# Kernel optimization log

Measured on AMD Instinct MI355X. Metric: run time of the kernel, lower is better.

The kernel has to match this reference:

```python
import jax, jax.numpy as jnp
import numpy as np
from jax import lax

T, B, R = 128, 128, 512  # timesteps, batch_size, read_size


def setup_inputs() -> dict:
    key = jax.random.key(0)
    ks = jax.random.split(key, 5)
    return {
        "u":  jax.random.uniform(ks[0], (T, B, 1), dtype=jnp.float32),
        "d1": jax.random.uniform(ks[1], (T, B, 1), dtype=jnp.float32),
        "d2": jax.random.uniform(ks[2], (T, B, 1), dtype=jnp.float32),
        "v1": jax.random.normal(ks[3], (T, B, R), dtype=jnp.float32),
        "v2": jax.random.normal(ks[4], (T, B, R), dtype=jnp.float32),
    }


def _forward(u, d1, d2, v1, v2):
    # Stack-style neural memory: each step pushes two (strength, value) slots,
    # reads up to total strength u from the top of the stack, then pops strength u.
    Tn, Bn, _ = u.shape
    Rn = v1.shape[-1]
    nslots = 2 * Tn
    # Pre-allocated slot store; unused slots have S=0, V=0 and contribute exactly 0
    # to both the read summary and strength_used, matching the growing-list semantics.
    S0 = jnp.zeros((nslots, Bn, 1), dtype=u.dtype)
    V0 = jnp.zeros((nslots, Bn, Rn), dtype=v1.dtype)

    def step(carry, inp):
        S, V = carry
        u_t, d1_t, d2_t, v1_t, v2_t, t = inp
        # push(d1, d2, v1, v2)
        S = S.at[2 * t].set(d1_t).at[2 * t + 1].set(d2_t)
        V = V.at[2 * t].set(v1_t).at[2 * t + 1].set(v2_t)
        Srev = S[::-1]  # stack order: top (most recent) first
        Vrev = V[::-1]

        # read(u): sequential scan over slots with strength bookkeeping
        def read_step(c, sv):
            summary, used = c
            s_i, v_i = sv
            # NOTE: torch.max(u - strength_used) is a GLOBAL max over the (B,1)
            # tensor (0-dim scalar), faithfully reproduced here.
            scal = jnp.max(u_t - used)
            summary = summary + v_i * jnp.minimum(s_i, scal)
            return (summary, used + s_i), None

        (summary, _), _ = lax.scan(
            read_step,
            (jnp.zeros((Bn, Rn), u.dtype), jnp.zeros((Bn, 1), u.dtype)),
            (Srev, Vrev),
        )

        # pop(u): elementwise strength depletion, same slot order
        def pop_step(used, s_i):
            s_new = s_i - jnp.minimum(s_i, jnp.maximum(jnp.zeros_like(s_i), u_t - used))
            return used + s_i, s_new

        _, Srev_new = lax.scan(pop_step, jnp.zeros((Bn, 1), u.dtype), Srev)
        return (Srev_new[::-1], V), summary

    xs = (u, d1, d2, v1, v2, jnp.arange(Tn))
    (_, _), outs = lax.scan(step, (S0, V0), xs)
    return outs  # (T, B, R) read contents per step


def reference(u, d1, d2, v1, v2):
    return _forward(u, d1, d2, v1, v2)
```

## Files before the change

kernel.cpp:

```cpp
#include <hip/hip_runtime.h>
#include <hip/hip_bf16.h>
#include <math.h>

constexpr int T = 128;
constexpr int B = 128;
constexpr int R = 512;
constexpr int NS = 256;

typedef __attribute__((ext_vector_type(8))) short bf16x8;
typedef __attribute__((ext_vector_type(4))) float f32x4;

static __device__ __forceinline__ ushort f2bf(float f) {
    union { float f; unsigned u; } v; v.f = f;
    unsigned r = v.u + 0x7fffu + ((v.u >> 16) & 1u);
    return (ushort)(r >> 16);
}

__global__ __launch_bounds__(512) void weights(
    const float* __restrict__ u, const float* __restrict__ d1,
    const float* __restrict__ d2, ushort* __restrict__ w)
{
    const int t    = blockIdx.x;
    const int tid  = threadIdx.x;
    const int wv   = tid >> 6;
    const int lane = tid & 63;
    __shared__ float eH[T][B];
    __shared__ float smin[8][B];

    const int nfl = t * B;
    for (int i = tid * 4; i < nfl; i += 2048) {
        const float4 a  = *(const float4*)(d1 + i);
        const float4 b4 = *(const float4*)(d2 + i);
        const float4 c4 = *(const float4*)(u + i);
        *(float4*)(&eH[0][0] + i) =
            make_float4(a.x + b4.x - c4.x, a.y + b4.y - c4.y,
                        a.z + b4.z - c4.z, a.w + b4.w - c4.w);
    }
    __syncthreads();

    if (tid < B) {
        float h = 0.f;
        #pragma unroll 4
        for (int tt = 0; tt < t; ++tt) {
            h = fmaxf(0.f, h + eH[tt][tid]);
            eH[tt][tid] = h;
        }
    }
    __syncthreads();

    const int b0 = lane, b1 = lane + 64;

    {
        const int rs = wv * 16;
        const int re = min(rs + 16, t);
        float sa = 1e30f, sb = 1e30f;
        for (int tau = rs; tau < re; ++tau) {
            sa = fminf(sa, eH[tau][b0]);
            sb = fminf(sb, eH[tau][b1]);
        }
        smin[wv][b0] = sa;
        smin[wv][b1] = sb;
    }
    __syncthreads();

    const float Ht1a = (t > 0) ? eH[t-1][b0] : 0.f;
    const float Ht1b = (t > 0) ? eH[t-1][b1] : 0.f;
    const float Hpa  = Ht1a + d1[t*B+b0] + d2[t*B+b0];
    const float Hpb  = Ht1b + d1[t*B+b1] + d2[t*B+b1];
    const float Aa   = u[t*B+b0] - Hpa;
    const float Ab   = u[t*B+b1] - Hpb;

    ushort* wrow0 = w + ((size_t)t * B + b0) * NS;
    ushort* wrow1 = w + ((size_t)t * B + b1) * NS;

    const int plo = wv * 16;
    if (plo <= t) {
        const int pe = min(plo + 15, t);
        float ma = 1e30f, mb = 1e30f;
        #pragma unroll
        for (int s = 0; s < 8; ++s) {
            if (s > wv) { ma = fminf(ma, smin[s][b0]); mb = fminf(mb, smin[s][b1]); }
        }
        float s2a = 0.f, s3a = 0.f, s2b = 0.f, s3b = 0.f;
        float nd1a = d1[pe*B+b0], nd1b = d1[pe*B+b1];
        float nd2a = d2[pe*B+b0], nd2b = d2[pe*B+b1];
        for (int p = pe; p >= plo; --p) {
            const float d1a = nd1a, d1b = nd1b, d2a = nd2a, d2b = nd2b;
            if (p > plo) {
                nd1a = d1[(p-1)*B+b0]; nd1b = d1[(p-1)*B+b1];
                nd2a = d2[(p-1)*B+b0]; nd2b = d2[(p-1)*B+b1];
            }
            if (p < t) { ma = fminf(ma, eH[p][b0]); mb = fminf(mb, eH[p][b1]); }
            const float basea = (p > 0) ? eH[p-1][b0] : 0.f;
            const float baseb = (p > 0) ? eH[p-1][b1] : 0.f;
            const float top0a = basea + d1a, top0b = baseb + d1b;
            const float top1a = top0a + d2a, top1b = top0b + d2b;

            const float sa0 = fminf(fmaxf(ma - basea, 0.f), d1a);
            const float sb0 = fminf(fmaxf(mb - baseb, 0.f), d1b);
            const float sa1 = fminf(fmaxf(ma - top0a, 0.f), d2a);
            const float sb1 = fminf(fmaxf(mb - top0b, 0.f), d2b);

            float cand0 = fmaxf(Aa + fminf(top0a, ma), Ab + fminf(top0b, mb));
            float cand1 = fmaxf(Aa + fminf(top1a, ma), Ab + fminf(top1b, mb));
            #pragma unroll
            for (int off = 32; off >= 1; off >>= 1) {
                cand0 = fmaxf(cand0, __shfl_xor(cand0, off));
                cand1 = fmaxf(cand1, __shfl_xor(cand1, off));
            }

            const float w0a = fminf(sa0, cand0), w0b = fminf(sb0, cand0);
            const float w1a = fminf(sa1, cand1), w1b = fminf(sb1, cand1);
            if (p & 1) { s2a = w0a; s3a = w1a; s2b = w0b; s3b = w1b; }
            else {
                const int g = p >> 1;
                *(ushort4*)(wrow0 + 4*g) =
                    make_ushort4(f2bf(w0a), f2bf(w1a), f2bf(s2a), f2bf(s3a));
                *(ushort4*)(wrow1 + 4*g) =
                    make_ushort4(f2bf(w0b), f2bf(w1b), f2bf(s2b), f2bf(s3b));
            }
        }
    }

    const int gstart = (t >> 1) + 1;
    const int ng = (NS / 4) - gstart;
    if (ng > 0) {
        const ushort4 z = make_ushort4(0, 0, 0, 0);
        const int total = ng * B;
        for (int idx = tid; idx < total; idx += 512) {
            const int gi = idx % ng;
            const int bb = idx / ng;
            *(ushort4*)(w + ((size_t)t*B + bb)*NS + 4*(gstart + gi)) = z;
        }
    }
}

#define RT 128
__global__ __launch_bounds__(512) void gemm_mfma(
    const ushort* __restrict__ w, const float* __restrict__ v1,
    const float* __restrict__ v2, float* __restrict__ out)
{
    const int b    = blockIdx.x;
    const int r0   = blockIdx.y * RT;
    const int tid  = threadIdx.x;
    const int wv   = tid >> 6;
    const int lane = tid & 63;

    __shared__ ushort As[2][128][40];
    __shared__ ushort Bs[2][128][40];

    const int arow = tid >> 2;
    const int ajh  = (tid & 3) * 8;
    const ushort* abase = w + ((size_t)arow * B + b) * NS + ajh;

    const int p2   = tid & 15;
    const int rseg = tid >> 4;
    const float* v1b = v1 + (size_t)b * R + r0 + rseg * 4;
    const float* v2b = v2 + (size_t)b * R + r0 + rseg * 4;

    f32x4 acc[8];
    const f32x4 zz = {0.f, 0.f, 0.f, 0.f};
    #pragma unroll
    for (int i = 0; i < 8; ++i) acc[i] = zz;

    uint4 la;
    float4 lv1, lv2;

    #define STAGE_LOAD(c) do {                                          \
        if (arow >= 16 * (c)) {                                         \
            la = *(const uint4*)(abase + (c) * 32);                     \
        } else {                                                        \
            la = make_uint4(0u, 0u, 0u, 0u);                            \
        }                                                               \
        const size_t off_ = (size_t)((c) * 16 + p2) * B * R;            \
        lv1 = *(const float4*)(v1b + off_);                             \
        lv2 = *(const float4*)(v2b + off_);                             \
    } while (0)

    #define STAGE_WRITE(buf) do {                                       \
        *(uint4*)&As[buf][arow][ajh] = la;                              \
        const float* f1_ = (const float*)&lv1;                          \
        const float* f2_ = (const float*)&lv2;                          \
        _Pragma("unroll")                                               \
        for (int i_ = 0; i_ < 4; ++i_) {                                \
            unsigned pk_ = (unsigned)f2bf(f1_[i_]) |                    \
                           ((unsigned)f2bf(f2_[i_]) << 16);             \
            *(unsigned*)&Bs[buf][rseg * 4 + i_][p2 * 2] = pk_;          \
        }                                                               \
    } while (0)

    const int tb = wv * 16 + (lane & 15);
    const int ko = (lane >> 4) * 8;

    STAGE_LOAD(0);
    STAGE_WRITE(0);
    #pragma unroll
    for (int c = 0; c < 8; ++c) {
        const int buf = c & 1;
        if (c < 7) STAGE_LOAD(c + 1);
        __syncthreads();
        if (c <= wv) {
            bf16x8 a0 = *(const bf16x8*)&As[buf][tb][ko];
            #pragma unroll
            for (int cf = 0; cf < 8; ++cf) {
                bf16x8 bb = *(const bf16x8*)&Bs[buf][cf*16 + (lane & 15)][ko];
                acc[cf] = __builtin_amdgcn_mfma_f32_16x16x32_bf16(a0, bb, acc[cf], 0, 0, 0);
            }
        }
        if (c < 7) STAGE_WRITE((c + 1) & 1);
    }

    const int dcol  = lane & 15;
    const int drow4 = (lane >> 4) * 4;
    #pragma unroll
    for (int cf = 0; cf < 8; ++cf) {
        const int rg = r0 + cf * 16 + dcol;
        #pragma unroll
        for (int i = 0; i < 4; ++i) {
            const int tg = wv * 16 + drow4 + i;
            out[((size_t)tg * B + b) * R + rg] = acc[cf][i];
        }
    }
    #undef STAGE_LOAD
    #undef STAGE_WRITE
}

extern "C" void kernel_launch(void* const* d_in, const int* in_sizes, int n_in,
                              void* d_out, int out_size, void* d_ws, size_t ws_size,
                              hipStream_t stream) {
    const float* u  = (const float*)d_in[0];
    const float* d1 = (const float*)d_in[1];
    const float* d2 = (const float*)d_in[2];
    const float* v1 = (const float*)d_in[3];
    const float* v2 = (const float*)d_in[4];
    float* out = (float*)d_out;
    ushort* w  = (ushort*)d_ws;

    weights<<<dim3(T), dim3(512), 0, stream>>>(u, d1, d2, w);
    gemm_mfma<<<dim3(B, R / RT), dim3(512), 0, stream>>>(w, v1, v2, out);
}
```

Measured before the change: 40.10 us.

## Precompute H recurrence with parallel prefix-scan kernel and halve GEMM R tile

Adds a separate kernel that computes the clamped running sum H for every batch column using a warp-level prefix sum and prefix min. Each weights block previously redid an O(t) serial scan in LDS, and that redundant work is removed. The weights kernel now reads H from global memory and keeps base values in rotating registers. The GEMM tile along R drops from 128 to 64, which doubles the block count, and each thread loads only v1 or v2 and drops the zero-fill guard on A loads. The costs are an extra launch, H traffic through global memory, and scalar 16-bit LDS stores. If the workspace is too small, H falls back to the output buffer.

Result: slower. 46.57 us (+16.1%).

```diff
diff --git a/kernel.cpp b/kernel.cpp
--- a/kernel.cpp
+++ b/kernel.cpp
@@ -16,37 +16,57 @@
     return (ushort)(r >> 16);
 }
 
+__global__ __launch_bounds__(128) void hscan(
+    const float* __restrict__ u, const float* __restrict__ d1,
+    const float* __restrict__ d2, float* __restrict__ H)
+{
+    const int b    = blockIdx.x * 2 + (threadIdx.x >> 6);
+    const int lane = threadIdx.x & 63;
+
+    int idx = lane * B + b;
+    float P = d1[idx] + d2[idx] - u[idx];
+    #pragma unroll
+    for (int off = 1; off < 64; off <<= 1) {
+        float o = __shfl_up(P, off);
+        if (lane >= off) P += o;
+    }
+    float M = P;
+    #pragma unroll
+    for (int off = 1; off < 64; off <<= 1) {
+        float o = __shfl_up(M, off);
+        if (lane >= off) M = fminf(M, o);
+    }
+    H[idx] = P - fminf(0.f, M);
+    const float carryP = __shfl(P, 63);
+    const float carryM = fminf(0.f, __shfl(M, 63));
+
+    idx = (64 + lane) * B + b;
+    float p2 = d1[idx] + d2[idx] - u[idx];
+    #pragma unroll
+    for (int off = 1; off < 64; off <<= 1) {
+        float o = __shfl_up(p2, off);
+        if (lane >= off) p2 += o;
+    }
+    float m2 = p2;
+    #pragma unroll
+    for (int off = 1; off < 64; off <<= 1) {
+        float o = __shfl_up(m2, off);
+        if (lane >= off) m2 = fminf(m2, o);
+    }
+    const float Pt = carryP + p2;
+    H[idx] = Pt - fminf(carryM, carryP + m2);
+}
+
 __global__ __launch_bounds__(512) void weights(
     const float* __restrict__ u, const float* __restrict__ d1,
-    const float* __restrict__ d2, ushort* __restrict__ w)
+    const float* __restrict__ d2, const float* __restrict__ H,
+    ushort* __restrict__ w)
 {
     const int t    = blockIdx.x;
     const int tid  = threadIdx.x;
     const int wv   = tid >> 6;
     const int lane = tid & 63;
-    __shared__ float eH[T][B];
     __shared__ float smin[8][B];
-
-    const int nfl = t * B;
-    for (int i = tid * 4; i < nfl; i += 2048) {
-        const float4 a  = *(const float4*)(d1 + i);
-        const float4 b4 = *(const float4*)(d2 + i);
-        const float4 c4 = *(const float4*)(u + i);
-        *(float4*)(&eH[0][0] + i) =
-            make_float4(a.x + b4.x - c4.x, a.y + b4.y - c4.y,
-                        a.z + b4.z - c4.z, a.w + b4.w - c4.w);
-    }
-    __syncthreads();
-
-    if (tid < B) {
-        float h = 0.f;
-        #pragma unroll 4
-        for (int tt = 0; tt < t; ++tt) {
-            h = fmaxf(0.f, h + eH[tt][tid]);
-            eH[tt][tid] = h;
-        }
-    }
-    __syncthreads();
 
     const int b0 = lane, b1 = lane + 64;
 
@@ -54,17 +74,18 @@
         const int rs = wv * 16;
         const int re = min(rs + 16, t);
         float sa = 1e30f, sb = 1e30f;
+        #pragma unroll 4
         for (int tau = rs; tau < re; ++tau) {
-            sa = fminf(sa, eH[tau][b0]);
-            sb = fminf(sb, eH[tau][b1]);
+            sa = fminf(sa, H[tau * B + b0]);
+            sb = fminf(sb, H[tau * B + b1]);
         }
         smin[wv][b0] = sa;
         smin[wv][b1] = sb;
     }
     __syncthreads();
 
-    const float Ht1a = (t > 0) ? eH[t-1][b0] : 0.f;
-    const float Ht1b = (t > 0) ? eH[t-1][b1] : 0.f;
+    const float Ht1a = (t > 0) ? H[(t-1)*B + b0] : 0.f;
+    const float Ht1b = (t > 0) ? H[(t-1)*B + b1] : 0.f;
     const float Hpa  = Ht1a + d1[t*B+b0] + d2[t*B+b0];
     const float Hpb  = Ht1b + d1[t*B+b1] + d2[t*B+b1];
     const float Aa   = u[t*B+b0] - Hpa;
@@ -81,18 +102,23 @@
         for (int s = 0; s < 8; ++s) {
             if (s > wv) { ma = fminf(ma, smin[s][b0]); mb = fminf(mb, smin[s][b1]); }
         }
-        float s2a = 0.f, s3a = 0.f, s2b = 0.f, s3b = 0.f;
+        float vala = (pe < t) ? H[pe*B + b0] : 0.f;
+        float valb = (pe < t) ? H[pe*B + b1] : 0.f;
+        float basea = (pe > 0) ? H[(pe-1)*B + b0] : 0.f;
+        float baseb = (pe > 0) ? H[(pe-1)*B + b1] : 0.f;
+        float pnb_a = (pe > 1) ? H[(pe-2)*B + b0] : 0.f;
+        float pnb_b = (pe > 1) ? H[(pe-2)*B + b1] : 0.f;
         float nd1a = d1[pe*B+b0], nd1b = d1[pe*B+b1];
         float nd2a = d2[pe*B+b0], nd2b = d2[pe*B+b1];
+        float s2a = 0.f, s3a = 0.f, s2b = 0.f, s3b = 0.f;
+
         for (int p = pe; p >= plo; --p) {
             const float d1a = nd1a, d1b = nd1b, d2a = nd2a, d2b = nd2b;
             if (p > plo) {
                 nd1a = d1[(p-1)*B+b0]; nd1b = d1[(p-1)*B+b1];
                 nd2a = d2[(p-1)*B+b0]; nd2b = d2[(p-1)*B+b1];
             }
-            if (p < t) { ma = fminf(ma, eH[p][b0]); mb = fminf(mb, eH[p][b1]); }
-            const float basea = (p > 0) ? eH[p-1][b0] : 0.f;
-            const float baseb = (p > 0) ? eH[p-1][b1] : 0.f;
+            if (p < t) { ma = fminf(ma, vala); mb = fminf(mb, valb); }
             const float top0a = basea + d1a, top0b = baseb + d1b;
             const float top1a = top0a + d2a, top1b = top0b + d2b;
 
@@ -119,6 +145,12 @@
                 *(ushort4*)(wrow1 + 4*g) =
                     make_ushort4(f2bf(w0b), f2bf(w1b), f2bf(s2b), f2bf(s3b));
             }
+            vala = basea; valb = baseb;
+            basea = pnb_a; baseb = pnb_b;
+            if (p - 2 >= plo) {
+                pnb_a = (p >= 3) ? H[(p-3)*B + b0] : 0.f;
+                pnb_b = (p >= 3) ? H[(p-3)*B + b1] : 0.f;
+            }
         }
     }
 
@@ -135,7 +167,7 @@
     }
 }
 
-#define RT 128
+#define RT 64
 __global__ __launch_bounds__(512) void gemm_mfma(
     const ushort* __restrict__ w, const float* __restrict__ v1,
     const float* __restrict__ v2, float* __restrict__ out)
@@ -147,46 +179,36 @@
     const int lane = tid & 63;
 
     __shared__ ushort As[2][128][40];
-    __shared__ ushort Bs[2][128][40];
+    __shared__ ushort Bs[2][RT][40];
 
     const int arow = tid >> 2;
     const int ajh  = (tid & 3) * 8;
     const ushort* abase = w + ((size_t)arow * B + b) * NS + ajh;
 
     const int p2   = tid & 15;
-    const int rseg = tid >> 4;
-    const float* v1b = v1 + (size_t)b * R + r0 + rseg * 4;
-    const float* v2b = v2 + (size_t)b * R + r0 + rseg * 4;
-
-    f32x4 acc[8];
+    const int rseg = (tid >> 4) & 15;
+    const int jodd = tid >> 8;
+    const float* vb = (jodd ? v2 : v1) + (size_t)b * R + r0 + rseg * 4;
+
+    f32x4 acc[4];
     const f32x4 zz = {0.f, 0.f, 0.f, 0.f};
     #pragma unroll
-    for (int i = 0; i < 8; ++i) acc[i] = zz;
+    for (int i = 0; i < 4; ++i) acc[i] = zz;
 
     uint4 la;
-    float4 lv1, lv2;
+    float4 lv;
 
     #define STAGE_LOAD(c) do {                                          \
-        if (arow >= 16 * (c)) {                                         \
-            la = *(const uint4*)(abase + (c) * 32);                     \
-        } else {                                                        \
-            la = make_uint4(0u, 0u, 0u, 0u);                            \
-        }                                                               \
-        const size_t off_ = (size_t)((c) * 16 + p2) * B * R;            \
-        lv1 = *(const float4*)(v1b + off_);                             \
-        lv2 = *(const float4*)(v2b + off_);                             \
+        la = *(const uint4*)(abase + (c) * 32);                         \
+        lv = *(const float4*)(vb + (size_t)((c) * 16 + p2) * B * R);    \
     } while (0)
 
     #define STAGE_WRITE(buf) do {                                       \
         *(uint4*)&As[buf][arow][ajh] = la;                              \
-        const float* f1_ = (const float*)&lv1;                          \
-        const float* f2_ = (const float*)&lv2;                          \
+        const float* f_ = (const float*)&lv;                            \
         _Pragma("unroll")                                               \
-        for (int i_ = 0; i_ < 4; ++i_) {                                \
-            unsigned pk_ = (unsigned)f2bf(f1_[i_]) |                    \
-                           ((unsigned)f2bf(f2_[i_]) << 16);             \
-            *(unsigned*)&Bs[buf][rseg * 4 + i_][p2 * 2] = pk_;          \
-        }                                                               \
+        for (int i_ = 0; i_ < 4; ++i_)                                  \
+            Bs[buf][rseg * 4 + i_][p2 * 2 + jodd] = f2bf(f_[i_]);       \
     } while (0)
 
     const int tb = wv * 16 + (lane & 15);
@@ -202,7 +224,7 @@
         if (c <= wv) {
             bf16x8 a0 = *(const bf16x8*)&As[buf][tb][ko];
             #pragma unroll
-            for (int cf = 0; cf < 8; ++cf) {
+            for (int cf = 0; cf < 4; ++cf) {
                 bf16x8 bb = *(const bf16x8*)&Bs[buf][cf*16 + (lane & 15)][ko];
                 acc[cf] = __builtin_amdgcn_mfma_f32_16x16x32_bf16(a0, bb, acc[cf], 0, 0, 0);
             }
@@ -213,7 +235,7 @@
     const int dcol  = lane & 15;
     const int drow4 = (lane >> 4) * 4;
     #pragma unroll
-    for (int cf = 0; cf < 8; ++cf) {
+    for (int cf = 0; cf < 4; ++cf) {
         const int rg = r0 + cf * 16 + dcol;
         #pragma unroll
         for (int i = 0; i < 4; ++i) {
@@ -234,8 +256,17 @@
     const float* v1 = (const float*)d_in[3];
     const float* v2 = (const float*)d_in[4];
     float* out = (float*)d_out;
-    ushort* w  = (ushort*)d_ws;
-
-    weights<<<dim3(T), dim3(512), 0, stream>>>(u, d1, d2, w);
+
+    const size_t welems = (size_t)T * B * NS;
+    ushort* w = (ushort*)d_ws;
+    float* H;
+    if (ws_size >= welems * sizeof(ushort) + (size_t)T * B * sizeof(float)) {
+        H = (float*)((char*)d_ws + welems * sizeof(ushort));
+    } else {
+        H = (float*)d_out;
+    }
+
+    hscan  <<<dim3(B / 2), dim3(128), 0, stream>>>(u, d1, d2, H);
+    weights<<<dim3(T),     dim3(512), 0, stream>>>(u, d1, d2, H, w);
     gemm_mfma<<<dim3(B, R / RT), dim3(512), 0, stream>>>(w, v1, v2, out);
 }
```
